# Optimization experiments

Hardware: AMD Instinct MI355X
Metric: run time of the kernel (lower is better)

The kernel has to match this reference:

```python
import jax, jax.numpy as jnp
import numpy as np

# Grid / camera constants (from repo config and hardcoded module values)
D = 256                 # FRUSTUM3D.GRID_DIMENSIONS = [256,256,256]
TRUNC = 3.0             # FRUSTUM3D.TRUNCATION (densify default for geometry)
VOX = 0.03              # voxel size (points *= 0.03)
H, W = 240, 320         # rendered image size (from plot_image ticks)
FX = FY = 240.0
CX, CY = 160.0, 120.0
CENTER = jnp.array([3.825, 3.825, 3.825], dtype=jnp.float32)
OFFSETS = jnp.array([[0.0, 0.0, 0.0], [0.8, 0.0, 0.15], [0.75, 0.0, 0.1], [-0.85, 0.0, 0.1]], dtype=jnp.float32)
ANGLES = jnp.array([0.0, 0.0, 0.3, 2.15], dtype=jnp.float32)
N_PTS = 2_000_000


def setup_inputs() -> dict:
    key = jax.random.key(0)
    k1, k2, k3, k4 = jax.random.split(key, 4)
    # unique voxel coordinates (sparse tensor coords are unique by construction)
    flat = jax.random.permutation(k1, D * D * D)[:N_PTS]
    ix = flat // (D * D)
    iy = (flat // D) % D
    iz = flat % D
    geo_coords = jnp.stack([ix, iy, iz], axis=1).astype(jnp.int32)
    geo_feats = (jax.random.uniform(k2, (N_PTS,)) * 2.0).astype(jnp.float32)  # ~half < 1.0 -> surface
    rgb_feats = jax.random.uniform(k3, (N_PTS, 3), dtype=jnp.float32)
    aux_views = jax.random.uniform(k4, (1, 4, 3, H, W), dtype=jnp.float32)
    # valid SE(3) poses: identity rotation, camera at z = -6 looking toward the volume
    T = np.eye(4, dtype=np.float32)
    T[2, 3] = -6.0
    cam_poses = jnp.asarray(np.stack([T] * 4)[None])  # [1,4,4,4]
    return {"geo_coords": geo_coords, "geo_feats": geo_feats, "rgb_feats": rgb_feats,
            "aux_views": aux_views, "cam_poses": cam_poses}


def _rot_y(a):
    ca, sa = jnp.cos(a), jnp.sin(a)
    return jnp.array([[ca, 0.0, sa], [0.0, 1.0, 0.0], [-sa, 0.0, ca]], dtype=jnp.float32)


def reference(geo_coords, geo_feats, rgb_feats, aux_views, cam_poses):
    ix, iy, iz = geo_coords[:, 0], geo_coords[:, 1], geo_coords[:, 2]
    # sparse -> dense densify (geometry default = truncation, rgb default = 0)
    dense_geo = jnp.full((D, D, D), TRUNC, dtype=geo_feats.dtype).at[ix, iy, iz].set(geo_feats)
    dense_rgb = jnp.zeros((D, D, D, 3), dtype=rgb_feats.dtype).at[ix, iy, iz].set(rgb_feats)
    # surface extraction: geometry < 1.0 (non-set voxels have value TRUNC >= 1 -> never surface,
    # so surface voxels are exactly the input coords with feat < 1; fixed-shape masked form)
    surf = dense_geo[ix, iy, iz] < 1.0                      # [N]
    pts_rgb = dense_rgb[ix, iy, iz]                         # [N,3]  (= rgb[:, surface_mask].T)
    points = geo_coords.astype(jnp.float32) * VOX - CENTER  # [N,3]

    def render(T, offset, angle):
        R = T[:3, :3] @ _rot_y(angle)
        c = T[:3, 3] + offset
        pc = (points - c) @ R                               # camera-frame points, [N,3]
        z = pc[:, 2]
        vis = surf & (z > 1e-4)
        zs = jnp.where(vis, z, 1.0)
        u = jnp.round(FX * pc[:, 0] / zs + CX).astype(jnp.int32)
        v = jnp.round(FY * pc[:, 1] / zs + CY).astype(jnp.int32)
        inb = vis & (u >= 0) & (u < W) & (v >= 0) & (v < H)
        flat = jnp.where(inb, v * W + u, H * W)             # H*W -> dropped
        depth = jnp.where(inb, z, jnp.inf)
        zbuf = jnp.full(H * W, jnp.inf, dtype=jnp.float32).at[flat].min(depth, mode='drop')
        win = inb & (depth <= zbuf[jnp.clip(flat, 0, H * W - 1)])
        wf = win.astype(pts_rgb.dtype)
        num = jnp.zeros((H * W, 3), dtype=pts_rgb.dtype).at[flat].add(pts_rgb * wf[:, None], mode='drop')
        cnt = jnp.zeros((H * W,), dtype=pts_rgb.dtype).at[flat].add(wf, mode='drop')
        return (num / jnp.maximum(cnt, 1.0)[:, None]).reshape(H, W, 3)

    imgs = jax.vmap(render)(cam_poses[0], OFFSETS, ANGLES)          # [4,H,W,3]
    views = jnp.transpose(aux_views[0], (0, 2, 3, 1))               # [4,H,W,3]
    mask = (imgs != 0.0).astype(imgs.dtype)                         # elementwise, like torch.where(img==0,0,1)
    n = 3.0 * jnp.sum(mask, axis=(1, 2, 3))                         # per-view N
    l = jnp.sum(jnp.abs(imgs * mask - views * mask), axis=(1, 2, 3))
    return jnp.sum(jnp.where(n > 0, l / jnp.maximum(n, 1.0), 0.0))
```

## Files before the change

### kernel.cpp

```cpp
#include <hip/hip_runtime.h>

#define HWPIX (240 * 320)
#define VWORDS (4 * HWPIX)
#define NBINS 960
#define NB 256
#define CAP 3000000
#define NBLD 1024
#define TBLD 1024
#define ITERS 2

__device__ __forceinline__ float dot3(float a0, float b0, float a1, float b1,
                                      float a2, float b2) {
  return __fadd_rn(__fadd_rn(__fmul_rn(a0, b0), __fmul_rn(a1, b1)),
                   __fmul_rn(a2, b2));
}

__device__ __forceinline__ bool project(const float* __restrict__ P, float px,
                                        float py, float pz, int& u, int& v,
                                        unsigned& zb) {
  float dx = __fsub_rn(px, P[9]);
  float dy = __fsub_rn(py, P[10]);
  float dz = __fsub_rn(pz, P[11]);
  float z = dot3(dx, P[2], dy, P[5], dz, P[8]);
  if (!(z > 1e-4f)) return false;
  float x = dot3(dx, P[0], dy, P[3], dz, P[6]);
  float y = dot3(dx, P[1], dy, P[4], dz, P[7]);
  u = (int)rintf(__fadd_rn(__fdiv_rn(__fmul_rn(240.0f, x), z), 160.0f));
  v = (int)rintf(__fadd_rn(__fdiv_rn(__fmul_rn(240.0f, y), z), 120.0f));
  if (u < 0 || u >= 320 || v < 0 || v >= 240) return false;
  zb = __float_as_uint(z);
  return true;
}

__device__ __forceinline__ void compute_params(const float* __restrict__ cam,
                                               float* __restrict__ params, int k) {
  const float offx[4] = {0.f, 0.8f, 0.75f, -0.85f};
  const float offy[4] = {0.f, 0.f, 0.f, 0.f};
  const float offz[4] = {0.f, 0.15f, 0.1f, 0.1f};
  const float angs[4] = {0.f, 0.f, 0.3f, 2.15f};
  const float* T = cam + k * 16;
  float ca = cosf(angs[k]);
  float sa = sinf(angs[k]);
  float Ry[3][3] = {{ca, 0.f, sa}, {0.f, 1.f, 0.f}, {-sa, 0.f, ca}};
  float* P = params + k * 16;
  for (int i = 0; i < 3; ++i)
    for (int j = 0; j < 3; ++j)
      P[i * 3 + j] = dot3(T[i * 4 + 0], Ry[0][j], T[i * 4 + 1], Ry[1][j],
                          T[i * 4 + 2], Ry[2][j]);
  P[9]  = __fadd_rn(T[3],  offx[k]);
  P[10] = __fadd_rn(T[7],  offy[k]);
  P[11] = __fadd_rn(T[11], offz[k]);
}


__global__ __launch_bounds__(1024) void k_init3(const float* __restrict__ cam,
                                                float* __restrict__ params,
                                                double* __restrict__ lacc,
                                                unsigned long long* __restrict__ macc,
                                                unsigned* __restrict__ bin_cnt) {
  int t = threadIdx.x;
  if (t < 4) {
    lacc[t] = 0.0;
    macc[t] = 0ull;
    compute_params(cam, params, t);
  }
  if (t < NBINS) bin_cnt[t] = 0u;
}

__global__ __launch_bounds__(TBLD) void k_build(const int* __restrict__ coords,
                                                const float* __restrict__ gfeat,
                                                const float* __restrict__ params,
                                                unsigned* __restrict__ bin_cnt,
                                                uint2* __restrict__ recs,
                                                unsigned maxper, int N) {
  __shared__ unsigned h[NBINS];
  for (int j = threadIdx.x; j < NBINS; j += TBLD) h[j] = 0u;
  __syncthreads();
  int chunk = (N + NBLD - 1) / NBLD;
  int lo = blockIdx.x * chunk, hi = min(N, lo + chunk);

  unsigned zb_c[ITERS][4];
  unsigned meta_c[ITERS][4];
#pragma unroll
  for (int it = 0; it < ITERS; ++it) {
#pragma unroll
    for (int k = 0; k < 4; ++k) { meta_c[it][k] = 0u; zb_c[it][k] = 0u; }
    int i = lo + (int)threadIdx.x + it * TBLD;
    if (i < hi && gfeat[i] < 1.0f) {
      float px = __fsub_rn(__fmul_rn((float)coords[3 * i + 0], 0.03f), 3.825f);
      float py = __fsub_rn(__fmul_rn((float)coords[3 * i + 1], 0.03f), 3.825f);
      float pz = __fsub_rn(__fmul_rn((float)coords[3 * i + 2], 0.03f), 3.825f);
#pragma unroll
      for (int k = 0; k < 4; ++k) {
        int u, v;
        unsigned zb;
        if (project(params + k * 16, px, py, pz, u, v, zb)) {
          unsigned bin = (unsigned)(k * 240 + v);
          atomicAdd(&h[bin], 1u);
          meta_c[it][k] = 0x80000000u | (bin << 9) | (unsigned)u;
          zb_c[it][k] = zb;
        }
      }
    }
  }
  __syncthreads();
  for (int j = threadIdx.x; j < NBINS; j += TBLD) {
    unsigned tot = h[j];
    unsigned base = tot ? atomicAdd(&bin_cnt[j], tot) : 0u;
    h[j] = (unsigned)j * maxper + base;
  }
  __syncthreads();
#pragma unroll
  for (int it = 0; it < ITERS; ++it) {
#pragma unroll
    for (int k = 0; k < 4; ++k) {
      unsigned m = meta_c[it][k];
      if (m & 0x80000000u) {
        unsigned bin = (m >> 9) & 1023u;
        unsigned u = m & 511u;
        int i = lo + (int)threadIdx.x + it * TBLD;
        unsigned slot = atomicAdd(&h[bin], 1u);
        if (slot < (bin + 1u) * maxper)
          recs[slot] = make_uint2(zb_c[it][k], ((unsigned)i << 9) | u);
      }
    }
  }
}

__global__ __launch_bounds__(320) void k_render3(const uint2* __restrict__ recs,
                                                 const unsigned* __restrict__ bin_cnt,
                                                 unsigned maxper,
                                                 const float* __restrict__ rgb,
                                                 const float* __restrict__ views,
                                                 double* __restrict__ lacc,
                                                 unsigned long long* __restrict__ macc) {
  int bin = blockIdx.x;
  int k = bin / 240, v = bin % 240;
  unsigned cnt_b = bin_cnt[bin];
  if (cnt_b > maxper) cnt_b = maxper;
  if (cnt_b == 0) return;
  unsigned base = (unsigned)bin * maxper;
  unsigned end = base + cnt_b;
  __shared__ unsigned zmin[320];
  __shared__ float num0[320], num1[320], num2[320], cnt[320];
  int t = threadIdx.x;
  zmin[t] = 0x7f800000u;
  num0[t] = num1[t] = num2[t] = cnt[t] = 0.f;
  __syncthreads();
  for (unsigned j = base + t; j < end; j += 320) {
    uint2 r = recs[j];
    atomicMin(&zmin[r.y & 511u], r.x);
  }
  __syncthreads();
  for (unsigned j = base + t; j < end; j += 320) {
    uint2 r = recs[j];
    unsigned u = r.y & 511u;
    if (r.x <= zmin[u]) {
      unsigned idx = r.y >> 9;
      atomicAdd(&num0[u], rgb[3 * idx + 0]);
      atomicAdd(&num1[u], rgb[3 * idx + 1]);
      atomicAdd(&num2[u], rgb[3 * idx + 2]);
      atomicAdd(&cnt[u], 1.0f);
    }
  }
  __syncthreads();
  float lsum = 0.f;
  unsigned mc = 0;
  {
    float denom = fmaxf(cnt[t], 1.0f);
    float i0 = __fdiv_rn(num0[t], denom);
    float i1 = __fdiv_rn(num1[t], denom);
    float i2 = __fdiv_rn(num2[t], denom);
    const float* vw = views + (size_t)(k * 3) * HWPIX + v * 320 + t;
    if (i0 != 0.f) { mc++; lsum += fabsf(__fsub_rn(i0, vw[0])); }
    if (i1 != 0.f) { mc++; lsum += fabsf(__fsub_rn(i1, vw[HWPIX])); }
    if (i2 != 0.f) { mc++; lsum += fabsf(__fsub_rn(i2, vw[2 * HWPIX])); }
  }
  for (int off = 32; off > 0; off >>= 1) {
    lsum += __shfl_down(lsum, off);
    mc += __shfl_down(mc, off);
  }
  __shared__ float sl[5];
  __shared__ unsigned sm[5];
  int lane = t & 63, wid = t >> 6;
  if (lane == 0) { sl[wid] = lsum; sm[wid] = mc; }
  __syncthreads();
  if (t == 0) {
    float L = 0.f;
    unsigned M = 0;
    for (int w = 0; w < 5; ++w) { L += sl[w]; M += sm[w]; }
    atomicAdd(&lacc[k], (double)L);
    atomicAdd(&macc[k], (unsigned long long)M);
  }
}


__global__ void k_init(const float* __restrict__ cam, float* __restrict__ params,
                       double* __restrict__ lacc, unsigned long long* __restrict__ macc) {
  int k = threadIdx.x;
  if (k >= 4) return;
  lacc[k] = 0.0;
  macc[k] = 0ull;
  compute_params(cam, params, k);
}

__global__ __launch_bounds__(1024) void k_count(const int* __restrict__ coords,
                                                const float* __restrict__ gfeat,
                                                const float* __restrict__ params,
                                                unsigned* __restrict__ hist, int N) {
  __shared__ unsigned h[NBINS];
  for (int j = threadIdx.x; j < NBINS; j += blockDim.x) h[j] = 0;
  __syncthreads();
  int chunk = (N + NB - 1) / NB;
  int lo = blockIdx.x * chunk, hi = min(N, lo + chunk);
  for (int i = lo + threadIdx.x; i < hi; i += blockDim.x) {
    if (!(gfeat[i] < 1.0f)) continue;
    float px = __fsub_rn(__fmul_rn((float)coords[3 * i + 0], 0.03f), 3.825f);
    float py = __fsub_rn(__fmul_rn((float)coords[3 * i + 1], 0.03f), 3.825f);
    float pz = __fsub_rn(__fmul_rn((float)coords[3 * i + 2], 0.03f), 3.825f);
#pragma unroll
    for (int k = 0; k < 4; ++k) {
      int u, v;
      unsigned zb;
      if (project(params + k * 16, px, py, pz, u, v, zb))
        atomicAdd(&h[k * 240 + v], 1u);
    }
  }
  __syncthreads();
  for (int j = threadIdx.x; j < NBINS; j += blockDim.x)
    hist[j * NB + blockIdx.x] = h[j];
}

__global__ __launch_bounds__(NB) void k_scan_bin(unsigned* __restrict__ hist,
                                                 unsigned* __restrict__ bin_tot) {
  __shared__ unsigned sc[NB];
  int b = blockIdx.x;
  int t = threadIdx.x;
  unsigned vin = hist[b * NB + t];
  sc[t] = vin;
  __syncthreads();
  for (int off = 1; off < NB; off <<= 1) {
    unsigned add = (t >= off) ? sc[t - off] : 0u;
    __syncthreads();
    sc[t] += add;
    __syncthreads();
  }
  hist[b * NB + t] = sc[t] - vin;
  if (t == NB - 1) bin_tot[b] = sc[t];
}

__global__ __launch_bounds__(1024) void k_scan_base(const unsigned* __restrict__ bin_tot,
                                                    unsigned* __restrict__ bin_base) {
  __shared__ unsigned sc[NBINS];
  int t = threadIdx.x;
  if (t < NBINS) sc[t] = bin_tot[t];
  __syncthreads();
  for (int off = 1; off < NBINS; off <<= 1) {
    unsigned add = (t < NBINS && t >= off) ? sc[t - off] : 0u;
    __syncthreads();
    if (t < NBINS) sc[t] += add;
    __syncthreads();
  }
  if (t < NBINS) bin_base[t] = sc[t] - bin_tot[t];
  if (t == 0) bin_base[NBINS] = sc[NBINS - 1];
}

__global__ __launch_bounds__(1024) void k_scatter(const int* __restrict__ coords,
                                                  const float* __restrict__ gfeat,
                                                  const float* __restrict__ params,
                                                  const unsigned* __restrict__ hist,
                                                  const unsigned* __restrict__ bin_base,
                                                  uint2* __restrict__ recs, int N) {
  __shared__ unsigned cur[NBINS];
  for (int j = threadIdx.x; j < NBINS; j += blockDim.x)
    cur[j] = bin_base[j] + hist[j * NB + blockIdx.x];
  __syncthreads();
  int chunk = (N + NB - 1) / NB;
  int lo = blockIdx.x * chunk, hi = min(N, lo + chunk);
  for (int i = lo + threadIdx.x; i < hi; i += blockDim.x) {
    if (!(gfeat[i] < 1.0f)) continue;
    float px = __fsub_rn(__fmul_rn((float)coords[3 * i + 0], 0.03f), 3.825f);
    float py = __fsub_rn(__fmul_rn((float)coords[3 * i + 1], 0.03f), 3.825f);
    float pz = __fsub_rn(__fmul_rn((float)coords[3 * i + 2], 0.03f), 3.825f);
#pragma unroll
    for (int k = 0; k < 4; ++k) {
      int u, v;
      unsigned zb;
      if (project(params + k * 16, px, py, pz, u, v, zb)) {
        unsigned slot = atomicAdd(&cur[k * 240 + v], 1u);
        if (slot < CAP)
          recs[slot] = make_uint2(zb, ((unsigned)i << 9) | (unsigned)u);
      }
    }
  }
}

__global__ __launch_bounds__(320) void k_render(const uint2* __restrict__ recs,
                                                const unsigned* __restrict__ bin_base,
                                                const float* __restrict__ rgb,
                                                const float* __restrict__ views,
                                                double* __restrict__ lacc,
                                                unsigned long long* __restrict__ macc) {
  int bin = blockIdx.x;
  int k = bin / 240, v = bin % 240;
  unsigned base = min(bin_base[bin], (unsigned)CAP);
  unsigned end = min(bin_base[bin + 1], (unsigned)CAP);
  if (end <= base) return;
  __shared__ unsigned zmin[320];
  __shared__ float num0[320], num1[320], num2[320], cnt[320];
  int t = threadIdx.x;
  zmin[t] = 0x7f800000u;
  num0[t] = num1[t] = num2[t] = cnt[t] = 0.f;
  __syncthreads();
  for (unsigned j = base + t; j < end; j += 320) {
    uint2 r = recs[j];
    atomicMin(&zmin[r.y & 511u], r.x);
  }
  __syncthreads();
  for (unsigned j = base + t; j < end; j += 320) {
    uint2 r = recs[j];
    unsigned u = r.y & 511u;
    if (r.x <= zmin[u]) {
      unsigned idx = r.y >> 9;
      atomicAdd(&num0[u], rgb[3 * idx + 0]);
      atomicAdd(&num1[u], rgb[3 * idx + 1]);
      atomicAdd(&num2[u], rgb[3 * idx + 2]);
      atomicAdd(&cnt[u], 1.0f);
    }
  }
  __syncthreads();
  float lsum = 0.f;
  unsigned mc = 0;
  {
    float denom = fmaxf(cnt[t], 1.0f);
    float i0 = __fdiv_rn(num0[t], denom);
    float i1 = __fdiv_rn(num1[t], denom);
    float i2 = __fdiv_rn(num2[t], denom);
    const float* vw = views + (size_t)(k * 3) * HWPIX + v * 320 + t;
    if (i0 != 0.f) { mc++; lsum += fabsf(__fsub_rn(i0, vw[0])); }
    if (i1 != 0.f) { mc++; lsum += fabsf(__fsub_rn(i1, vw[HWPIX])); }
    if (i2 != 0.f) { mc++; lsum += fabsf(__fsub_rn(i2, vw[2 * HWPIX])); }
  }
  for (int off = 32; off > 0; off >>= 1) {
    lsum += __shfl_down(lsum, off);
    mc += __shfl_down(mc, off);
  }
  __shared__ float sl[5];
  __shared__ unsigned sm[5];
  int lane = t & 63, wid = t >> 6;
  if (lane == 0) { sl[wid] = lsum; sm[wid] = mc; }
  __syncthreads();
  if (t == 0) {
    float L = 0.f;
    unsigned M = 0;
    for (int w = 0; w < 5; ++w) { L += sl[w]; M += sm[w]; }
    atomicAdd(&lacc[k], (double)L);
    atomicAdd(&macc[k], (unsigned long long)M);
  }
}

__global__ void k_final(const double* __restrict__ lacc,
                        const unsigned long long* __restrict__ macc,
                        float* __restrict__ out) {
  float total = 0.f;
  for (int k = 0; k < 4; ++k) {
    float n = 3.0f * (float)macc[k];
    float l = (float)lacc[k];
    if (n > 0.f) total += __fdiv_rn(l, fmaxf(n, 1.0f));
  }
  out[0] = total;
}

__global__ void kf_init(unsigned* __restrict__ zbuf, float* __restrict__ num,
                        float* __restrict__ cnt) {
  int i = blockIdx.x * blockDim.x + threadIdx.x;
  int stride = gridDim.x * blockDim.x;
  for (int j = i; j < VWORDS; j += stride) {
    zbuf[j] = 0x7f800000u;
    cnt[j] = 0.f;
  }
  for (int j = i; j < 3 * VWORDS; j += stride) num[j] = 0.f;
}

__global__ void kf_zmin(const int* __restrict__ coords, const float* __restrict__ gfeat,
                        const float* __restrict__ params, unsigned* __restrict__ zbuf,
                        int N) {
  int i = blockIdx.x * blockDim.x + threadIdx.x;
  if (i >= N) return;
  if (!(gfeat[i] < 1.0f)) return;
  float px = __fsub_rn(__fmul_rn((float)coords[3 * i + 0], 0.03f), 3.825f);
  float py = __fsub_rn(__fmul_rn((float)coords[3 * i + 1], 0.03f), 3.825f);
  float pz = __fsub_rn(__fmul_rn((float)coords[3 * i + 2], 0.03f), 3.825f);
#pragma unroll
  for (int k = 0; k < 4; ++k) {
    int u, v;
    unsigned zb;
    if (project(params + k * 16, px, py, pz, u, v, zb))
      atomicMin(&zbuf[k * HWPIX + v * 320 + u], zb);
  }
}

__global__ void kf_accum(const int* __restrict__ coords, const float* __restrict__ gfeat,
                         const float* __restrict__ rgb, const float* __restrict__ params,
                         const unsigned* __restrict__ zbuf, float* __restrict__ num,
                         float* __restrict__ cnt, int N) {
  int i = blockIdx.x * blockDim.x + threadIdx.x;
  if (i >= N) return;
  if (!(gfeat[i] < 1.0f)) return;
  float px = __fsub_rn(__fmul_rn((float)coords[3 * i + 0], 0.03f), 3.825f);
  float py = __fsub_rn(__fmul_rn((float)coords[3 * i + 1], 0.03f), 3.825f);
  float pz = __fsub_rn(__fmul_rn((float)coords[3 * i + 2], 0.03f), 3.825f);
#pragma unroll
  for (int k = 0; k < 4; ++k) {
    int u, v;
    unsigned zb;
    if (project(params + k * 16, px, py, pz, u, v, zb)) {
      int g = k * HWPIX + v * 320 + u;
      if (zb <= zbuf[g]) {
        atomicAdd(&num[g * 3 + 0], rgb[3 * i + 0]);
        atomicAdd(&num[g * 3 + 1], rgb[3 * i + 1]);
        atomicAdd(&num[g * 3 + 2], rgb[3 * i + 2]);
        atomicAdd(&cnt[g], 1.0f);
      }
    }
  }
}

__global__ void kf_loss(const float* __restrict__ num, const float* __restrict__ cnt,
                        const float* __restrict__ views, double* __restrict__ lacc,
                        unsigned long long* __restrict__ macc) {
  int k = blockIdx.y;
  int p = blockIdx.x * blockDim.x + threadIdx.x;
  float lsum = 0.f;
  unsigned mc = 0;
  if (p < HWPIX) {
    int fl = k * HWPIX + p;
    float denom = fmaxf(cnt[fl], 1.0f);
#pragma unroll
    for (int ch = 0; ch < 3; ++ch) {
      float img = __fdiv_rn(num[fl * 3 + ch], denom);
      if (img != 0.0f) {
        mc++;
        lsum += fabsf(__fsub_rn(img, views[(k * 3 + ch) * HWPIX + p]));
      }
    }
  }
  for (int off = 32; off > 0; off >>= 1) {
    lsum += __shfl_down(lsum, off);
    mc += __shfl_down(mc, off);
  }
  __shared__ float sl[4];
  __shared__ unsigned sm[4];
  int lane = threadIdx.x & 63, wid = threadIdx.x >> 6;
  if (lane == 0) { sl[wid] = lsum; sm[wid] = mc; }
  __syncthreads();
  if (threadIdx.x == 0) {
    atomicAdd(&lacc[k], (double)(sl[0] + sl[1] + sl[2] + sl[3]));
    atomicAdd(&macc[k], (unsigned long long)(sm[0] + sm[1] + sm[2] + sm[3]));
  }
}

extern "C" void kernel_launch(void* const* d_in, const int* in_sizes, int n_in,
                              void* d_out, int out_size, void* d_ws, size_t ws_size,
                              hipStream_t stream) {
  const int* coords = (const int*)d_in[0];
  const float* gfeat = (const float*)d_in[1];
  const float* rgb = (const float*)d_in[2];
  const float* views = (const float*)d_in[3];
  const float* cam = (const float*)d_in[4];
  int N = in_sizes[0] / 3;

  char* ws = (char*)d_ws;
  double* lacc = (double*)ws;
  unsigned long long* macc = (unsigned long long*)(ws + 32);
  float* params = (float*)(ws + 128);
  unsigned* bin_cnt = (unsigned*)(ws + 512);
  const size_t T1_HDR = 65536;

  size_t maxper = 0;
  if (ws_size > T1_HDR) maxper = (ws_size - T1_HDR) / ((size_t)NBINS * 8);
  if (maxper > 131072) maxper = 131072;
  if (maxper >= 30720 && (long long)N <= (long long)NBLD * TBLD * ITERS) {
    uint2* recs = (uint2*)(ws + T1_HDR);
    k_init3<<<1, 1024, 0, stream>>>(cam, params, lacc, macc, bin_cnt);
    k_build<<<NBLD, TBLD, 0, stream>>>(coords, gfeat, params, bin_cnt, recs,
                                       (unsigned)maxper, N);
    k_render3<<<NBINS, 320, 0, stream>>>(recs, bin_cnt, (unsigned)maxper, rgb,
                                         views, lacc, macc);
    k_final<<<1, 1, 0, stream>>>(lacc, macc, (float*)d_out);
    return;
  }

  const size_t HDR = 512 + 4096;
  const size_t HIST_B = (size_t)NBINS * NB * 4;
  const size_t TOT_B = (size_t)NBINS * 4;
  const size_t BASE_B = 4096;
  const size_t REC_B = (size_t)CAP * 8;
  const size_t need_fast = HDR + HIST_B + TOT_B + BASE_B + REC_B;

  if (ws_size >= need_fast) {
    unsigned* hist = (unsigned*)(ws + HDR);
    unsigned* bin_tot = (unsigned*)(ws + HDR + HIST_B);
    unsigned* bin_base = (unsigned*)(ws + HDR + HIST_B + TOT_B);
    uint2* recs = (uint2*)(ws + HDR + HIST_B + TOT_B + BASE_B);
    k_init<<<1, 64, 0, stream>>>(cam, params, lacc, macc);
    k_count<<<NB, 1024, 0, stream>>>(coords, gfeat, params, hist, N);
    k_scan_bin<<<NBINS, NB, 0, stream>>>(hist, bin_tot);
    k_scan_base<<<1, 1024, 0, stream>>>(bin_tot, bin_base);
    k_scatter<<<NB, 1024, 0, stream>>>(coords, gfeat, params, hist, bin_base, recs, N);
    k_render<<<NBINS, 320, 0, stream>>>(recs, bin_base, rgb, views, lacc, macc);
    k_final<<<1, 1, 0, stream>>>(lacc, macc, (float*)d_out);
  } else {
    unsigned* zbuf = (unsigned*)(ws + HDR);
    float* cnt = (float*)(ws + HDR + (size_t)VWORDS * 4);
    float* num = (float*)(ws + HDR + (size_t)VWORDS * 8);
    k_init<<<1, 64, 0, stream>>>(cam, params, lacc, macc);
    kf_init<<<1024, 256, 0, stream>>>(zbuf, num, cnt);
    int blocks = (N + 255) / 256;
    kf_zmin<<<blocks, 256, 0, stream>>>(coords, gfeat, params, zbuf, N);
    kf_accum<<<blocks, 256, 0, stream>>>(coords, gfeat, rgb, params, zbuf, num, cnt, N);
    kf_loss<<<dim3((HWPIX + 255) / 256, 4), 256, 0, stream>>>(num, cnt, views, lacc, macc);
    k_final<<<1, 1, 0, stream>>>(lacc, macc, (float*)d_out);
  }
}
```

Measured before the change: 67.80 us.

## Replace shared-memory bin histogram with replicated global atomic counters

The build kernel no longer does a per-block shared-memory histogram, prefix reservation and second scatter pass. Each surface point now reserves its slot directly through a global atomicAdd on one of 8 replicated per-bin counters chosen by block index, and each bin's record space is split into 8 sub-regions. This removes two block-wide syncs and the register-cached two-phase scatter, using a grid-stride loop with smaller blocks. In exchange it adds global atomic contention, spread across replicas, and the render kernel must read 8 counters and walk 8 sub-ranges per bin. Each replica also has less capacity before records are dropped.

```diff
diff --git a/kernel.cpp b/kernel.cpp
--- a/kernel.cpp
+++ b/kernel.cpp
@@ -5,9 +5,9 @@
 #define NBINS 960
 #define NB 256
 #define CAP 3000000
-#define NBLD 1024
-#define TBLD 1024
-#define ITERS 2
+#define REP 8
+#define NBLD 2048
+#define TBLD 256
 
 __device__ __forceinline__ float dot3(float a0, float b0, float a1, float b1,
                                       float a2, float b2) {
@@ -64,7 +64,7 @@
     macc[t] = 0ull;
     compute_params(cam, params, t);
   }
-  if (t < NBINS) bin_cnt[t] = 0u;
+  for (int j = t; j < REP * NBINS; j += 1024) bin_cnt[j] = 0u;
 }
 
 __global__ __launch_bounds__(TBLD) void k_build(const int* __restrict__ coords,
@@ -73,55 +73,24 @@
                                                 unsigned* __restrict__ bin_cnt,
                                                 uint2* __restrict__ recs,
                                                 unsigned maxper, int N) {
-  __shared__ unsigned h[NBINS];
-  for (int j = threadIdx.x; j < NBINS; j += TBLD) h[j] = 0u;
-  __syncthreads();
-  int chunk = (N + NBLD - 1) / NBLD;
-  int lo = blockIdx.x * chunk, hi = min(N, lo + chunk);
-
-  unsigned zb_c[ITERS][4];
-  unsigned meta_c[ITERS][4];
-#pragma unroll
-  for (int it = 0; it < ITERS; ++it) {
-#pragma unroll
-    for (int k = 0; k < 4; ++k) { meta_c[it][k] = 0u; zb_c[it][k] = 0u; }
-    int i = lo + (int)threadIdx.x + it * TBLD;
-    if (i < hi && gfeat[i] < 1.0f) {
-      float px = __fsub_rn(__fmul_rn((float)coords[3 * i + 0], 0.03f), 3.825f);
-      float py = __fsub_rn(__fmul_rn((float)coords[3 * i + 1], 0.03f), 3.825f);
-      float pz = __fsub_rn(__fmul_rn((float)coords[3 * i + 2], 0.03f), 3.825f);
-#pragma unroll
-      for (int k = 0; k < 4; ++k) {
-        int u, v;
-        unsigned zb;
-        if (project(params + k * 16, px, py, pz, u, v, zb)) {
-          unsigned bin = (unsigned)(k * 240 + v);
-          atomicAdd(&h[bin], 1u);
-          meta_c[it][k] = 0x80000000u | (bin << 9) | (unsigned)u;
-          zb_c[it][k] = zb;
-        }
-      }
-    }
-  }
-  __syncthreads();
-  for (int j = threadIdx.x; j < NBINS; j += TBLD) {
-    unsigned tot = h[j];
-    unsigned base = tot ? atomicAdd(&bin_cnt[j], tot) : 0u;
-    h[j] = (unsigned)j * maxper + base;
-  }
-  __syncthreads();
-#pragma unroll
-  for (int it = 0; it < ITERS; ++it) {
+  unsigned rep = (unsigned)blockIdx.x & (REP - 1);
+  unsigned sub = maxper / REP;
+  int stride = gridDim.x * blockDim.x;
+  for (int i = blockIdx.x * blockDim.x + threadIdx.x; i < N; i += stride) {
+    if (!(gfeat[i] < 1.0f)) continue;
+    float px = __fsub_rn(__fmul_rn((float)coords[3 * i + 0], 0.03f), 3.825f);
+    float py = __fsub_rn(__fmul_rn((float)coords[3 * i + 1], 0.03f), 3.825f);
+    float pz = __fsub_rn(__fmul_rn((float)coords[3 * i + 2], 0.03f), 3.825f);
 #pragma unroll
     for (int k = 0; k < 4; ++k) {
-      unsigned m = meta_c[it][k];
-      if (m & 0x80000000u) {
-        unsigned bin = (m >> 9) & 1023u;
-        unsigned u = m & 511u;
-        int i = lo + (int)threadIdx.x + it * TBLD;
-        unsigned slot = atomicAdd(&h[bin], 1u);
-        if (slot < (bin + 1u) * maxper)
-          recs[slot] = make_uint2(zb_c[it][k], ((unsigned)i << 9) | u);
+      int u, v;
+      unsigned zb;
+      if (project(params + k * 16, px, py, pz, u, v, zb)) {
+        unsigned bin = (unsigned)(k * 240 + v);
+        unsigned off = atomicAdd(&bin_cnt[rep * NBINS + bin], 1u);
+        if (off < sub)
+          recs[(size_t)bin * maxper + rep * sub + off] =
+              make_uint2(zb, ((unsigned)i << 9) | (unsigned)u);
       }
     }
   }
@@ -136,31 +105,44 @@
                                                  unsigned long long* __restrict__ macc) {
   int bin = blockIdx.x;
   int k = bin / 240, v = bin % 240;
-  unsigned cnt_b = bin_cnt[bin];
-  if (cnt_b > maxper) cnt_b = maxper;
-  if (cnt_b == 0) return;
-  unsigned base = (unsigned)bin * maxper;
-  unsigned end = base + cnt_b;
+  unsigned sub = maxper / REP;
+  unsigned c_r[REP];
+  unsigned tot = 0;
+#pragma unroll
+  for (int r = 0; r < REP; ++r) {
+    unsigned c = bin_cnt[r * NBINS + bin];
+    c_r[r] = c < sub ? c : sub;
+    tot += c_r[r];
+  }
+  if (tot == 0) return;
   __shared__ unsigned zmin[320];
   __shared__ float num0[320], num1[320], num2[320], cnt[320];
   int t = threadIdx.x;
   zmin[t] = 0x7f800000u;
   num0[t] = num1[t] = num2[t] = cnt[t] = 0.f;
   __syncthreads();
-  for (unsigned j = base + t; j < end; j += 320) {
-    uint2 r = recs[j];
-    atomicMin(&zmin[r.y & 511u], r.x);
-  }
-  __syncthreads();
-  for (unsigned j = base + t; j < end; j += 320) {
-    uint2 r = recs[j];
-    unsigned u = r.y & 511u;
-    if (r.x <= zmin[u]) {
-      unsigned idx = r.y >> 9;
-      atomicAdd(&num0[u], rgb[3 * idx + 0]);
-      atomicAdd(&num1[u], rgb[3 * idx + 1]);
-      atomicAdd(&num2[u], rgb[3 * idx + 2]);
-      atomicAdd(&cnt[u], 1.0f);
+#pragma unroll
+  for (int r = 0; r < REP; ++r) {
+    unsigned b0 = (unsigned)bin * maxper + r * sub;
+    for (unsigned j = b0 + t; j < b0 + c_r[r]; j += 320) {
+      uint2 rec = recs[j];
+      atomicMin(&zmin[rec.y & 511u], rec.x);
+    }
+  }
+  __syncthreads();
+#pragma unroll
+  for (int r = 0; r < REP; ++r) {
+    unsigned b0 = (unsigned)bin * maxper + r * sub;
+    for (unsigned j = b0 + t; j < b0 + c_r[r]; j += 320) {
+      uint2 rec = recs[j];
+      unsigned u = rec.y & 511u;
+      if (rec.x <= zmin[u]) {
+        unsigned idx = rec.y >> 9;
+        atomicAdd(&num0[u], rgb[3 * idx + 0]);
+        atomicAdd(&num1[u], rgb[3 * idx + 1]);
+        atomicAdd(&num2[u], rgb[3 * idx + 2]);
+        atomicAdd(&cnt[u], 1.0f);
+      }
     }
   }
   __syncthreads();
@@ -480,7 +462,8 @@
   size_t maxper = 0;
   if (ws_size > T1_HDR) maxper = (ws_size - T1_HDR) / ((size_t)NBINS * 8);
   if (maxper > 131072) maxper = 131072;
-  if (maxper >= 30720 && (long long)N <= (long long)NBLD * TBLD * ITERS) {
+  maxper &= ~(size_t)(REP - 1);
+  if (maxper >= 30720 && N <= 0x7FFFFF) {
     uint2* recs = (uint2*)(ws + T1_HDR);
     k_init3<<<1, 1024, 0, stream>>>(cam, params, lacc, macc, bin_cnt);
     k_build<<<NBLD, TBLD, 0, stream>>>(coords, gfeat, params, bin_cnt, recs,
```

Result: slower. 198.4 us (+192.6%).

## Compute z-buffer minimum with global atomics during build, drop render min pass

Applied to the files above, without the earlier changes.

Moves the per-pixel depth minimum out of the render kernel. The build kernel now does a global atomicMin into a full-size z-buffer as it scatters records, and the init kernel, widened to many blocks, fills that buffer with infinity. The render kernel loads the precomputed minimum and no longer makes a first pass over its records, which saves one read of the record stream. In exchange it adds about a million global atomics in build plus a 1.2MB buffer initialisation and read.

```diff
diff --git a/kernel.cpp b/kernel.cpp
--- a/kernel.cpp
+++ b/kernel.cpp
@@ -53,24 +53,31 @@
 }
 
 
-__global__ __launch_bounds__(1024) void k_init3(const float* __restrict__ cam,
-                                                float* __restrict__ params,
-                                                double* __restrict__ lacc,
-                                                unsigned long long* __restrict__ macc,
-                                                unsigned* __restrict__ bin_cnt) {
+__global__ __launch_bounds__(256) void k_init3(const float* __restrict__ cam,
+                                               float* __restrict__ params,
+                                               double* __restrict__ lacc,
+                                               unsigned long long* __restrict__ macc,
+                                               unsigned* __restrict__ bin_cnt,
+                                               unsigned* __restrict__ zbuf) {
   int t = threadIdx.x;
-  if (t < 4) {
-    lacc[t] = 0.0;
-    macc[t] = 0ull;
-    compute_params(cam, params, t);
-  }
-  if (t < NBINS) bin_cnt[t] = 0u;
+  if (blockIdx.x == 0) {
+    if (t < 4) {
+      lacc[t] = 0.0;
+      macc[t] = 0ull;
+      compute_params(cam, params, t);
+    }
+    for (int j = t; j < NBINS; j += 256) bin_cnt[j] = 0u;
+  }
+  int i = blockIdx.x * 256 + t;
+  int stride = gridDim.x * 256;
+  for (int j = i; j < VWORDS; j += stride) zbuf[j] = 0x7f800000u;
 }
 
 __global__ __launch_bounds__(TBLD) void k_build(const int* __restrict__ coords,
                                                 const float* __restrict__ gfeat,
                                                 const float* __restrict__ params,
                                                 unsigned* __restrict__ bin_cnt,
+                                                unsigned* __restrict__ zbuf,
                                                 uint2* __restrict__ recs,
                                                 unsigned maxper, int N) {
   __shared__ unsigned h[NBINS];
@@ -119,6 +126,7 @@
         unsigned bin = (m >> 9) & 1023u;
         unsigned u = m & 511u;
         int i = lo + (int)threadIdx.x + it * TBLD;
+        atomicMin(&zbuf[bin * 320 + u], zb_c[it][k]);
         unsigned slot = atomicAdd(&h[bin], 1u);
         if (slot < (bin + 1u) * maxper)
           recs[slot] = make_uint2(zb_c[it][k], ((unsigned)i << 9) | u);
@@ -129,6 +137,7 @@
 
 __global__ __launch_bounds__(320) void k_render3(const uint2* __restrict__ recs,
                                                  const unsigned* __restrict__ bin_cnt,
+                                                 const unsigned* __restrict__ zbuf,
                                                  unsigned maxper,
                                                  const float* __restrict__ rgb,
                                                  const float* __restrict__ views,
@@ -144,13 +153,8 @@
   __shared__ unsigned zmin[320];
   __shared__ float num0[320], num1[320], num2[320], cnt[320];
   int t = threadIdx.x;
-  zmin[t] = 0x7f800000u;
+  zmin[t] = zbuf[bin * 320 + t];
   num0[t] = num1[t] = num2[t] = cnt[t] = 0.f;
-  __syncthreads();
-  for (unsigned j = base + t; j < end; j += 320) {
-    uint2 r = recs[j];
-    atomicMin(&zmin[r.y & 511u], r.x);
-  }
   __syncthreads();
   for (unsigned j = base + t; j < end; j += 320) {
     uint2 r = recs[j];
@@ -475,18 +479,19 @@
   unsigned long long* macc = (unsigned long long*)(ws + 32);
   float* params = (float*)(ws + 128);
   unsigned* bin_cnt = (unsigned*)(ws + 512);
-  const size_t T1_HDR = 65536;
+  unsigned* zbuf1 = (unsigned*)(ws + 65536);
+  const size_t T1_REC = 65536 + 1310720;
 
   size_t maxper = 0;
-  if (ws_size > T1_HDR) maxper = (ws_size - T1_HDR) / ((size_t)NBINS * 8);
+  if (ws_size > T1_REC) maxper = (ws_size - T1_REC) / ((size_t)NBINS * 8);
   if (maxper > 131072) maxper = 131072;
   if (maxper >= 30720 && (long long)N <= (long long)NBLD * TBLD * ITERS) {
-    uint2* recs = (uint2*)(ws + T1_HDR);
-    k_init3<<<1, 1024, 0, stream>>>(cam, params, lacc, macc, bin_cnt);
-    k_build<<<NBLD, TBLD, 0, stream>>>(coords, gfeat, params, bin_cnt, recs,
-                                       (unsigned)maxper, N);
-    k_render3<<<NBINS, 320, 0, stream>>>(recs, bin_cnt, (unsigned)maxper, rgb,
-                                         views, lacc, macc);
+    uint2* recs = (uint2*)(ws + T1_REC);
+    k_init3<<<256, 256, 0, stream>>>(cam, params, lacc, macc, bin_cnt, zbuf1);
+    k_build<<<NBLD, TBLD, 0, stream>>>(coords, gfeat, params, bin_cnt, zbuf1,
+                                       recs, (unsigned)maxper, N);
+    k_render3<<<NBINS, 320, 0, stream>>>(recs, bin_cnt, zbuf1, (unsigned)maxper,
+                                         rgb, views, lacc, macc);
     k_final<<<1, 1, 0, stream>>>(lacc, macc, (float*)d_out);
     return;
   }
```

Measured after the change: 134.7 us. 1.99x slower.
